# Optimization experiments

Hardware: AMD Instinct MI355X
Metric: run time of the kernel (lower is better)

The kernel has to match this reference:

```python
import jax, jax.numpy as jnp
import numpy as np

GRID = 2
SPAN = 2.0
EMBED = 64
HIDDEN = 128
PRED_LEN = 12
N = 1024
T = 8
SCENE_SIZE = 64


def _social_pool(ht, pos, scene, active):
    """ht: [N,H], pos: [N,2], scene: [N] int, active: [N] bool -> [N, GRID*GRID, H].
    Vectorized equivalent of the per-scene scatter_add pooling: pairwise mask over
    same-scene, active, within-area, non-self pairs; bin neighbor hidden states."""
    n = ht.shape[0]
    half = SPAN / 2.0
    eps = 0.01
    rel = pos[None, :, :] - pos[:, None, :]  # rel[i,j] = pos_j - pos_i
    within = ((rel[..., 0] < half - eps) & (rel[..., 0] > -half + eps)
              & (rel[..., 1] < half - eps) & (rel[..., 1] > -half + eps))
    pair = (within & (~jnp.eye(n, dtype=bool))
            & (scene[:, None] == scene[None, :])
            & active[:, None] & active[None, :])
    cell = SPAN / GRID
    gidx = jnp.floor((rel + half) / cell).astype(jnp.int32)
    gid = jnp.clip(gidx[..., 0] * GRID + gidx[..., 1], 0, GRID * GRID - 1)
    onehot = jax.nn.one_hot(gid, GRID * GRID, dtype=ht.dtype) * pair[..., None].astype(ht.dtype)
    # pooled[i,g,h] = sum_j onehot[i,j,g] * ht[j,h]
    return jnp.einsum('ijg,jh->igh', onehot, ht)


def _lstm_step(x, h, c, Wih, Whh, bih, bhh):
    z = x @ Wih.T + bih + h @ Whh.T + bhh
    i, f, g, o = jnp.split(z, 4, axis=-1)
    c_new = jax.nn.sigmoid(f) * c + jax.nn.sigmoid(i) * jnp.tanh(g)
    h_new = jax.nn.sigmoid(o) * jnp.tanh(c_new)
    return h_new, c_new


def setup_inputs() -> dict:
    key = jax.random.key(0)
    ks = jax.random.split(key, 16)
    past_traj = jax.random.uniform(ks[0], (N, T, 2), dtype=jnp.float32) * 8.0
    past_traj_rel = jax.random.normal(ks[1], (N, T, 2), dtype=jnp.float32)
    past_traj_timestamp_mask = jnp.ones((N, T), dtype=jnp.int32)
    is_predictable = jnp.ones((N, 1), dtype=jnp.int32)
    same_scene_mask = (jnp.arange(N, dtype=jnp.int32) // SCENE_SIZE).reshape(N, 1)

    def lin(k, fan_out, fan_in):
        b = 1.0 / np.sqrt(fan_in)
        return jax.random.uniform(k, (fan_out, fan_in), jnp.float32, -b, b)

    pos_W = lin(ks[2], EMBED, 2)
    pos_b = jnp.zeros((EMBED,), jnp.float32)
    soc_W = lin(ks[3], EMBED, GRID * GRID * HIDDEN)
    soc_b = jnp.zeros((EMBED,), jnp.float32)
    Wih = lin(ks[4], 4 * HIDDEN, 2 * EMBED)
    Whh = lin(ks[5], 4 * HIDDEN, HIDDEN)
    bih = jnp.zeros((4 * HIDDEN,), jnp.float32)
    bhh = jnp.zeros((4 * HIDDEN,), jnp.float32)
    h0 = jax.random.normal(ks[6], (HIDDEN,), jnp.float32) * 0.1
    c0 = jax.random.normal(ks[7], (HIDDEN,), jnp.float32) * 0.1
    pred_W = lin(ks[8], 5, HIDDEN)
    pred_b = jnp.zeros((5,), jnp.float32)
    return {
        'past_traj': past_traj, 'past_traj_rel': past_traj_rel,
        'past_traj_timestamp_mask': past_traj_timestamp_mask,
        'is_predictable': is_predictable, 'same_scene_mask': same_scene_mask,
        'pos_W': pos_W, 'pos_b': pos_b, 'soc_W': soc_W, 'soc_b': soc_b,
        'Wih': Wih, 'Whh': Whh, 'bih': bih, 'bhh': bhh,
        'h0': h0, 'c0': c0, 'pred_W': pred_W, 'pred_b': pred_b,
    }


def reference(past_traj, past_traj_rel, past_traj_timestamp_mask, is_predictable,
              same_scene_mask, pos_W, pos_b, soc_W, soc_b, Wih, Whh, bih, bhh,
              h0, c0, pred_W, pred_b):
    n = past_traj.shape[0]
    scene = same_scene_mask[:, 0]
    ht = jnp.broadcast_to(h0[None, :], (n, HIDDEN))
    ct = jnp.broadcast_to(c0[None, :], (n, HIDDEN))

    def obs_step(carry, inp):
        ht, ct = carry
        point, rel, m = inp  # [N,2], [N,2], [N]
        active = m == 1
        pooled = _social_pool(ht, point, scene, active)  # [N,G^2,H]
        et = jax.nn.relu(rel @ pos_W.T + pos_b)
        at = jax.nn.relu(pooled.reshape(n, -1) @ soc_W.T + soc_b)
        x = jnp.concatenate([et, at], axis=-1)
        h_new, c_new = _lstm_step(x, ht, ct, Wih, Whh, bih, bhh)
        ht = jnp.where(active[:, None], h_new, ht)
        ct = jnp.where(active[:, None], c_new, ct)
        return (ht, ct), None

    obs_inp = (jnp.moveaxis(past_traj, 1, 0), jnp.moveaxis(past_traj_rel, 1, 0),
               jnp.moveaxis(past_traj_timestamp_mask, 1, 0))
    (ht, ct), _ = jax.lax.scan(obs_step, (ht, ct), obs_inp)

    pred_active = past_traj_timestamp_mask[:, -1] == 1
    pos0 = past_traj[:, -1, :]

    def pred_step(carry, _):
        ht, ct, pos = carry
        out = ht @ pred_W.T + pred_b  # [N,5]
        rel = out[:, :2]
        pos = pos + rel
        pooled = _social_pool(ht, pos, scene, pred_active)
        et = jax.nn.relu(rel @ pos_W.T + pos_b)
        at = jax.nn.relu(pooled.reshape(n, -1) @ soc_W.T + soc_b)
        x = jnp.concatenate([et, at], axis=-1)
        h_new, c_new = _lstm_step(x, ht, ct, Wih, Whh, bih, bhh)
        ht = jnp.where(pred_active[:, None], h_new, ht)
        ct = jnp.where(pred_active[:, None], c_new, ct)
        return (ht, ct, pos), (out, pos)

    (_, _, _), (outs, trajs) = jax.lax.scan(pred_step, (ht, ct, pos0), None, length=PRED_LEN)
    pred_out_all = jnp.where(pred_active[:, None, None], jnp.moveaxis(outs, 0, 1), 0.0)
    pred_traj_all = jnp.where(pred_active[:, None, None], jnp.moveaxis(trajs, 0, 1), 0.0)
    # is_predictable is all-ones in this setup, so the final boolean filter is identity
    return pred_out_all, pred_traj_all
```

## Files before the change

kernel.cpp:

```cpp
#include <hip/hip_runtime.h>

#define NAGENT 64
#define HID    128
#define TOBS   8
#define PREDL  12
#define NTHR   1024
#define XP     264
#define PP     264
#define SP2    264

typedef __attribute__((ext_vector_type(8))) short bf16x8;
typedef __attribute__((ext_vector_type(4))) short bf16x4;
typedef __attribute__((ext_vector_type(4))) float f32x4;
typedef __attribute__((ext_vector_type(2))) unsigned int u32x2;

__device__ __forceinline__ unsigned short f2bf(float f) {
    unsigned int x = __float_as_uint(f);
    unsigned int r = (x + 0x7fffu + ((x >> 16) & 1u)) >> 16;
    return (unsigned short)r;
}
__device__ __forceinline__ float bf2f(unsigned short u) {
    return __uint_as_float(((unsigned int)u) << 16);
}
__device__ __forceinline__ float sigmf(float x) {
    return __builtin_amdgcn_rcpf(1.0f + __expf(-x));
}
__device__ __forceinline__ float tanhf_fast(float x) {
    x = fminf(fmaxf(x, -15.0f), 15.0f);
    float e = __expf(2.0f * x);
    return (e - 1.0f) * __builtin_amdgcn_rcpf(e + 1.0f);
}
__device__ __forceinline__ float sel4(float a0, float a1, float a2, float a3, int k) {
    float lo = (k & 1) ? a1 : a0;
    float hi = (k & 1) ? a3 : a2;
    return (k & 2) ? hi : lo;
}

__global__ void prep_weights(const float* __restrict__ Wih, const float* __restrict__ Whh,
                             const float* __restrict__ socW, const float* __restrict__ predW,
                             unsigned short* __restrict__ wd, unsigned short* __restrict__ wb,
                             unsigned short* __restrict__ wp) {
    int idx = blockIdx.x * 256 + threadIdx.x;
    if (idx < 131072) {
        int e = idx & 7, l = (idx >> 3) & 63, t = idx >> 9;
        int kt = t & 7, nt = t >> 3;
        int k = kt * 32 + ((l >> 4) << 3) + e;
        int n = nt * 16 + (l & 15);
        int d = n >> 2, g = n & 3;
        int row = g * 128 + d;
        float v = (k < 128) ? Wih[row * 128 + k] : Whh[row * 128 + (k - 128)];
        wd[idx] = f2bf(v);
    } else if (idx < 163840) {
        int i2 = idx - 131072;
        int e = i2 & 7, l = (i2 >> 3) & 63, t = i2 >> 9;
        int kt = t & 3, nt = t >> 2;
        int k = kt * 32 + ((l >> 4) << 3) + e;
        int r = nt * 16 + (l & 15);
        int eo = r >> 2, g = r & 3;
        wb[i2] = f2bf(socW[eo * 512 + g * 128 + k]);
    } else if (idx < 167936) {
        int i3 = idx - 163840;
        int e = i3 & 7, l = (i3 >> 3) & 63, f = i3 >> 9;
        int kt = f & 3, half = f >> 2;
        int k = kt * 32 + ((l >> 4) << 3) + e;
        int n = l & 15;
        float v = (n < 5) ? predW[n * 128 + k] : 0.0f;
        unsigned short hi = f2bf(v);
        wp[i3] = half ? f2bf(v - bf2f(hi)) : hi;
    }
}

__global__ __launch_bounds__(NTHR) void social_lstm_mfma(
    const float* __restrict__ past_traj, const float* __restrict__ past_traj_rel,
    const int* __restrict__ ts_mask, const int* __restrict__ scene_in,
    const float* __restrict__ pos_W, const float* __restrict__ pos_b,
    const float* __restrict__ soc_b,
    const float* __restrict__ bih, const float* __restrict__ bhh,
    const float* __restrict__ h0, const float* __restrict__ c0,
    const float* __restrict__ pred_b,
    const unsigned short* __restrict__ wd, const unsigned short* __restrict__ wb,
    const unsigned short* __restrict__ wp,
    float* __restrict__ out)
{
    __shared__ __align__(16) unsigned short sh_X[NAGENT][XP];
    __shared__ __align__(16) unsigned short sh_P[NAGENT][PP];
    __shared__ __align__(16) unsigned short sh_S[NAGENT][SP2];
    __shared__ float sh_px[NAGENT], sh_py[NAGENT], sh_rx[NAGENT], sh_ry[NAGENT];
    __shared__ float sh_o[5][NAGENT];
    __shared__ int   sh_act[NAGENT], sh_scene[NAGENT];

    const int tid  = threadIdx.x;
    const int lane = tid & 63;
    const int wv   = __builtin_amdgcn_readfirstlane(tid >> 6);
    const int gbase = blockIdx.x * NAGENT;
    const int c16 = lane & 15;
    const int q4  = lane >> 4;
    const int go  = c16 & 3;
    const int dq  = c16 >> 2;

    float bs[2], c_st[4][2], hnew[4][2];
    int dimv[2];
    #pragma unroll
    for (int s = 0; s < 2; ++s) {
        const int n = (2 * wv + s) * 16 + c16;
        const int d = n >> 2, g = n & 3;
        bs[s] = bih[g * 128 + d] + bhh[g * 128 + d];
        dimv[s] = (2 * wv + s) * 4 + dq;
        #pragma unroll
        for (int mj = 0; mj < 4; ++mj) c_st[mj][s] = c0[dimv[s]];
    }
    for (int p = tid; p < NAGENT * HID; p += NTHR) {
        int a = p >> 7, d = p & 127;
        sh_X[a][128 + d] = f2bf(h0[d]);
    }
    if (tid < NAGENT) sh_scene[tid] = scene_in[gbase + tid];
    __syncthreads();

    const bf16x8* wdp = (const bf16x8*)wd + (2 * wv * 8) * 64 + lane;
    const bf16x8* wbp = (const bf16x8*)wb + (wv * 4) * 64 + lane;
    const unsigned short* xaD = &sh_X[c16][q4 * 8];
    const unsigned short* xaB = &sh_X[c16][128 + q4 * 8];

    for (int step = 0; step < TOBS + PREDL; ++step) {
        if (step < TOBS) {
            if (tid < NAGENT) {
                const int ig = gbase + tid;
                sh_px[tid] = past_traj[(ig * TOBS + step) * 2 + 0];
                sh_py[tid] = past_traj[(ig * TOBS + step) * 2 + 1];
                sh_rx[tid] = past_traj_rel[(ig * TOBS + step) * 2 + 0];
                sh_ry[tid] = past_traj_rel[(ig * TOBS + step) * 2 + 1];
                sh_act[tid] = (ts_mask[ig * TOBS + step] == 1) ? 1 : 0;
            }
        } else {
            if (wv < 4) {
                const bf16x8* wpv = (const bf16x8*)wp;
                f32x4 pa = (f32x4){0.f, 0.f, 0.f, 0.f};
                #pragma unroll
                for (int kt = 0; kt < 4; ++kt) {
                    const bf16x8 a = *(const bf16x8*)&sh_X[wv * 16 + c16][128 + kt * 32 + q4 * 8];
                    pa = __builtin_amdgcn_mfma_f32_16x16x32_bf16(a, wpv[kt * 64 + lane], pa, 0, 0, 0);
                    pa = __builtin_amdgcn_mfma_f32_16x16x32_bf16(a, wpv[(4 + kt) * 64 + lane], pa, 0, 0, 0);
                }
                if (c16 < 5) {
                    const float pb = pred_b[c16];
                    #pragma unroll
                    for (int rr = 0; rr < 4; ++rr)
                        sh_o[c16][wv * 16 + q4 * 4 + rr] = pa[rr] + pb;
                }
            }
            __syncthreads();
            if (tid < NAGENT) {
                const int i = tid;
                const float rx = sh_o[0][i], ry = sh_o[1][i];
                const float px = sh_px[i] + rx, py = sh_py[i] + ry;
                sh_px[i] = px; sh_py[i] = py;
                sh_rx[i] = rx; sh_ry[i] = ry;
                const float m = sh_act[i] ? 1.0f : 0.0f;
                const int p = step - TOBS;
                const int ig = gbase + i;
                float* po = out + (ig * PREDL + p) * 5;
                #pragma unroll
                for (int q = 0; q < 5; ++q) po[q] = m * sh_o[q][i];
                float* pt = out + 61440 + (ig * PREDL + p) * 2;
                pt[0] = m * px; pt[1] = m * py;
            }
        }
        __syncthreads();

        #pragma unroll
        for (int it = 0; it < 4; ++it) {
            const int p = it * NTHR + tid;
            const int i = p >> 6, j = p & 63;
            const float dx = sh_px[j] - sh_px[i];
            const float dy = sh_py[j] - sh_py[i];
            const bool within = (dx < 0.99f) & (dx > -0.99f) & (dy < 0.99f) & (dy > -0.99f);
            const bool pair = within && (i != j) && (sh_scene[i] == sh_scene[j])
                              && sh_act[i] && sh_act[j];
            const int gid = ((dx >= 0.f) ? 2 : 0) + ((dy >= 0.f) ? 1 : 0);
            unsigned int w0 = 0, w1 = 0;
            if (pair) {
                if (gid == 0) w0 = 0x3f80u;
                else if (gid == 1) w0 = 0x3f800000u;
                else if (gid == 2) w1 = 0x3f80u;
                else w1 = 0x3f800000u;
            }
            u32x2 w; w[0] = w0; w[1] = w1;
            *(u32x2*)&sh_P[i][j * 4] = w;
        }
        {
            const float rx = sh_rx[lane], ry = sh_ry[lane];
            const int e0 = wv * 4;
            #pragma unroll
            for (int u = 0; u < 4; ++u) {
                const int e = e0 + u;
                sh_X[lane][e] = f2bf(fmaxf(pos_b[e] + rx * pos_W[e * 2] + ry * pos_W[e * 2 + 1], 0.f));
            }
        }
        {
            f32x4 acc2[4];
            #pragma unroll
            for (int mj = 0; mj < 4; ++mj) acc2[mj] = (f32x4){0.f, 0.f, 0.f, 0.f};
            #pragma unroll
            for (int kt = 0; kt < 4; ++kt) {
                const bf16x8 b = wbp[kt * 64];
                #pragma unroll
                for (int mj = 0; mj < 4; ++mj) {
                    const bf16x8 a = *(const bf16x8*)(xaB + mj * 16 * XP + kt * 32);
                    acc2[mj] = __builtin_amdgcn_mfma_f32_16x16x32_bf16(a, b, acc2[mj], 0, 0, 0);
                }
            }
            const int rcol = wv * 16 + c16;
            #pragma unroll
            for (int mj = 0; mj < 4; ++mj)
                #pragma unroll
                for (int rr = 0; rr < 4; ++rr)
                    sh_S[mj * 16 + q4 * 4 + rr][rcol] = f2bf(acc2[mj][rr]);
        }
        __syncthreads();

        {
            const int mt = wv & 3, nt = wv >> 2;
            const int cb = 4 * (nt * 16 + c16);
            f32x4 cac = (f32x4){0.f, 0.f, 0.f, 0.f};
            #pragma unroll
            for (int kt = 0; kt < 8; ++kt) {
                const bf16x8 a = *(const bf16x8*)&sh_P[mt * 16 + c16][kt * 32 + q4 * 8];
                const int j0 = kt * 8 + q4 * 2;
                const bf16x4 lo = *(const bf16x4*)&sh_S[j0][cb];
                const bf16x4 hi = *(const bf16x4*)&sh_S[j0 + 1][cb];
                const bf16x8 b = __builtin_shufflevector(lo, hi, 0, 1, 2, 3, 4, 5, 6, 7);
                cac = __builtin_amdgcn_mfma_f32_16x16x32_bf16(a, b, cac, 0, 0, 0);
            }
            const int e = nt * 16 + c16;
            const float sb = soc_b[e];
            #pragma unroll
            for (int rr = 0; rr < 4; ++rr)
                sh_X[mt * 16 + q4 * 4 + rr][64 + e] = f2bf(fmaxf(cac[rr] + sb, 0.f));
        }
        __syncthreads();

        {
            f32x4 acc[4][2];
            #pragma unroll
            for (int mj = 0; mj < 4; ++mj) {
                acc[mj][0] = (f32x4){0.f, 0.f, 0.f, 0.f};
                acc[mj][1] = (f32x4){0.f, 0.f, 0.f, 0.f};
            }
            #pragma unroll 2
            for (int kt = 0; kt < 8; ++kt) {
                const bf16x8 b0 = wdp[kt * 64];
                const bf16x8 b1 = wdp[kt * 64 + 512];
                #pragma unroll
                for (int mj = 0; mj < 4; ++mj) {
                    const bf16x8 a = *(const bf16x8*)(xaD + mj * 16 * XP + kt * 32);
                    acc[mj][0] = __builtin_amdgcn_mfma_f32_16x16x32_bf16(a, b0, acc[mj][0], 0, 0, 0);
                    acc[mj][1] = __builtin_amdgcn_mfma_f32_16x16x32_bf16(a, b1, acc[mj][1], 0, 0, 0);
                }
            }
            #pragma unroll
            for (int mj = 0; mj < 4; ++mj) {
                const int a = mj * 16 + q4 * 4 + go;
                const bool act = sh_act[a] != 0;
                #pragma unroll
                for (int s = 0; s < 2; ++s) {
                    const float z0 = acc[mj][s][0] + bs[s];
                    const float z1 = acc[mj][s][1] + bs[s];
                    const float z2 = acc[mj][s][2] + bs[s];
                    const float z3 = acc[mj][s][3] + bs[s];
                    const float s0 = sel4(z0, z1, z2, z3, go);
                    const float s1 = sel4(z0, z1, z2, z3, go ^ 1);
                    const float s2 = sel4(z0, z1, z2, z3, go ^ 2);
                    const float s3 = sel4(z0, z1, z2, z3, go ^ 3);
                    const float t1 = __shfl_xor(s1, 1, 64);
                    const float t2 = __shfl_xor(s2, 2, 64);
                    const float t3 = __shfl_xor(s3, 3, 64);
                    const float zi = sel4(s0, t1, t2, t3, go);
                    const float zf = sel4(s0, t1, t2, t3, go ^ 1);
                    const float zg = sel4(s0, t1, t2, t3, go ^ 2);
                    const float zo = sel4(s0, t1, t2, t3, go ^ 3);
                    const float cold = c_st[mj][s];
                    const float cn = sigmf(zf) * cold + sigmf(zi) * tanhf_fast(zg);
                    const float hn = sigmf(zo) * tanhf_fast(cn);
                    c_st[mj][s] = act ? cn : cold;
                    const float hold = bf2f(sh_X[a][128 + dimv[s]]);
                    hnew[mj][s] = act ? hn : hold;
                }
            }
        }
        __syncthreads();
        #pragma unroll
        for (int mj = 0; mj < 4; ++mj) {
            const int a = mj * 16 + q4 * 4 + go;
            sh_X[a][128 + dimv[0]] = f2bf(hnew[mj][0]);
            sh_X[a][128 + dimv[1]] = f2bf(hnew[mj][1]);
        }
        __syncthreads();
    }
}

extern "C" void kernel_launch(void* const* d_in, const int* in_sizes, int n_in,
                              void* d_out, int out_size, void* d_ws, size_t ws_size,
                              hipStream_t stream) {
    (void)in_sizes; (void)n_in; (void)out_size; (void)ws_size;
    unsigned short* wd = (unsigned short*)d_ws;
    unsigned short* wb = wd + 131072;
    unsigned short* wp = wb + 32768;
    prep_weights<<<656, 256, 0, stream>>>(
        (const float*)d_in[9], (const float*)d_in[10],
        (const float*)d_in[7], (const float*)d_in[15], wd, wb, wp);
    social_lstm_mfma<<<16, NTHR, 0, stream>>>(
        (const float*)d_in[0],
        (const float*)d_in[1],
        (const int*)  d_in[2],
        (const int*)  d_in[4],
        (const float*)d_in[5],
        (const float*)d_in[6],
        (const float*)d_in[8],
        (const float*)d_in[11],
        (const float*)d_in[12],
        (const float*)d_in[13],
        (const float*)d_in[14],
        (const float*)d_in[16],
        wd, wb, wp,
        (float*)d_out);
}
```

Before: 290.2 us.

## Double-buffer hidden state and positions to remove per-step barriers

Splits the hidden state into a double-buffered array so the new h can be written directly after the gate math, dropping the extra barrier and register staging. Position, velocity and activity arrays are double-buffered too, and the next observed step's inputs are prefetched at the end of the current step. The prediction-head writes and position update move into the MFMA waves, removing a separate single-wave phase and another barrier. This adds shared memory and index bookkeeping, and the active-mask handling during prediction relies on buffer 1 holding the last observed mask.

```diff
diff --git a/kernel.cpp b/kernel.cpp
--- a/kernel.cpp
+++ b/kernel.cpp
@@ -5,13 +5,14 @@
 #define TOBS   8
 #define PREDL  12
 #define NTHR   1024
-#define XP     264
+#define XH     136
 #define PP     264
-#define SP2    264
+#define SPP    268
 
 typedef __attribute__((ext_vector_type(8))) short bf16x8;
 typedef __attribute__((ext_vector_type(4))) short bf16x4;
 typedef __attribute__((ext_vector_type(4))) float f32x4;
+typedef __attribute__((ext_vector_type(4))) int   i32x4;
 typedef __attribute__((ext_vector_type(2))) unsigned int u32x2;
 
 __device__ __forceinline__ unsigned short f2bf(float f) {
@@ -82,12 +83,14 @@
     const unsigned short* __restrict__ wp,
     float* __restrict__ out)
 {
-    __shared__ __align__(16) unsigned short sh_X[NAGENT][XP];
+    __shared__ __align__(16) unsigned short sh_X[NAGENT][XH];
+    __shared__ __align__(16) unsigned short sh_H[2][NAGENT][XH];
     __shared__ __align__(16) unsigned short sh_P[NAGENT][PP];
-    __shared__ __align__(16) unsigned short sh_S[NAGENT][SP2];
-    __shared__ float sh_px[NAGENT], sh_py[NAGENT], sh_rx[NAGENT], sh_ry[NAGENT];
-    __shared__ float sh_o[5][NAGENT];
-    __shared__ int   sh_act[NAGENT], sh_scene[NAGENT];
+    __shared__ __align__(16) unsigned short sh_S[NAGENT][SPP];
+    __shared__ float sh_px[2][NAGENT], sh_py[2][NAGENT];
+    __shared__ float sh_rx[2][NAGENT], sh_ry[2][NAGENT];
+    __shared__ __align__(16) int sh_act[2][NAGENT];
+    __shared__ int sh_scene[NAGENT];
 
     const int tid  = threadIdx.x;
     const int lane = tid & 63;
@@ -98,7 +101,7 @@
     const int go  = c16 & 3;
     const int dq  = c16 >> 2;
 
-    float bs[2], c_st[4][2], hnew[4][2];
+    float bs[2], c_st[4][2];
     int dimv[2];
     #pragma unroll
     for (int s = 0; s < 2; ++s) {
@@ -111,71 +114,73 @@
     }
     for (int p = tid; p < NAGENT * HID; p += NTHR) {
         int a = p >> 7, d = p & 127;
-        sh_X[a][128 + d] = f2bf(h0[d]);
-    }
-    if (tid < NAGENT) sh_scene[tid] = scene_in[gbase + tid];
+        sh_H[0][a][d] = f2bf(h0[d]);
+    }
+    if (tid < NAGENT) {
+        const int ig = gbase + tid;
+        sh_scene[tid] = scene_in[ig];
+        sh_px[0][tid] = past_traj[(ig * TOBS + 0) * 2 + 0];
+        sh_py[0][tid] = past_traj[(ig * TOBS + 0) * 2 + 1];
+        sh_rx[0][tid] = past_traj_rel[(ig * TOBS + 0) * 2 + 0];
+        sh_ry[0][tid] = past_traj_rel[(ig * TOBS + 0) * 2 + 1];
+        sh_act[0][tid] = (ts_mask[ig * TOBS + 0] == 1) ? 1 : 0;
+    }
     __syncthreads();
 
     const bf16x8* wdp = (const bf16x8*)wd + (2 * wv * 8) * 64 + lane;
     const bf16x8* wbp = (const bf16x8*)wb + (wv * 4) * 64 + lane;
-    const unsigned short* xaD = &sh_X[c16][q4 * 8];
-    const unsigned short* xaB = &sh_X[c16][128 + q4 * 8];
 
     for (int step = 0; step < TOBS + PREDL; ++step) {
-        if (step < TOBS) {
-            if (tid < NAGENT) {
-                const int ig = gbase + tid;
-                sh_px[tid] = past_traj[(ig * TOBS + step) * 2 + 0];
-                sh_py[tid] = past_traj[(ig * TOBS + step) * 2 + 1];
-                sh_rx[tid] = past_traj_rel[(ig * TOBS + step) * 2 + 0];
-                sh_ry[tid] = past_traj_rel[(ig * TOBS + step) * 2 + 1];
-                sh_act[tid] = (ts_mask[ig * TOBS + step] == 1) ? 1 : 0;
-            }
-        } else {
+        const int pb = step & 1;
+        const int hb = step & 1;
+        const int ab = (step < TOBS) ? pb : 1;
+
+        if (step >= TOBS) {
             if (wv < 4) {
                 const bf16x8* wpv = (const bf16x8*)wp;
                 f32x4 pa = (f32x4){0.f, 0.f, 0.f, 0.f};
                 #pragma unroll
                 for (int kt = 0; kt < 4; ++kt) {
-                    const bf16x8 a = *(const bf16x8*)&sh_X[wv * 16 + c16][128 + kt * 32 + q4 * 8];
+                    const bf16x8 a = *(const bf16x8*)&sh_H[hb][wv * 16 + c16][kt * 32 + q4 * 8];
                     pa = __builtin_amdgcn_mfma_f32_16x16x32_bf16(a, wpv[kt * 64 + lane], pa, 0, 0, 0);
                     pa = __builtin_amdgcn_mfma_f32_16x16x32_bf16(a, wpv[(4 + kt) * 64 + lane], pa, 0, 0, 0);
                 }
                 if (c16 < 5) {
-                    const float pb = pred_b[c16];
+                    const float pbias = pred_b[c16];
+                    const int p = step - TOBS;
+                    const int pprev = (step - 1) & 1;
                     #pragma unroll
-                    for (int rr = 0; rr < 4; ++rr)
-                        sh_o[c16][wv * 16 + q4 * 4 + rr] = pa[rr] + pb;
+                    for (int rr = 0; rr < 4; ++rr) {
+                        const int a = wv * 16 + q4 * 4 + rr;
+                        const float o = pa[rr] + pbias;
+                        const float m = sh_act[1][a] ? 1.0f : 0.0f;
+                        const int ig = gbase + a;
+                        out[(ig * PREDL + p) * 5 + c16] = m * o;
+                        if (c16 == 0) {
+                            const float px = sh_px[pprev][a] + o;
+                            sh_px[pb][a] = px; sh_rx[pb][a] = o;
+                            out[61440 + (ig * PREDL + p) * 2 + 0] = m * px;
+                        }
+                        if (c16 == 1) {
+                            const float py = sh_py[pprev][a] + o;
+                            sh_py[pb][a] = py; sh_ry[pb][a] = o;
+                            out[61440 + (ig * PREDL + p) * 2 + 1] = m * py;
+                        }
+                    }
                 }
             }
             __syncthreads();
-            if (tid < NAGENT) {
-                const int i = tid;
-                const float rx = sh_o[0][i], ry = sh_o[1][i];
-                const float px = sh_px[i] + rx, py = sh_py[i] + ry;
-                sh_px[i] = px; sh_py[i] = py;
-                sh_rx[i] = rx; sh_ry[i] = ry;
-                const float m = sh_act[i] ? 1.0f : 0.0f;
-                const int p = step - TOBS;
-                const int ig = gbase + i;
-                float* po = out + (ig * PREDL + p) * 5;
-                #pragma unroll
-                for (int q = 0; q < 5; ++q) po[q] = m * sh_o[q][i];
-                float* pt = out + 61440 + (ig * PREDL + p) * 2;
-                pt[0] = m * px; pt[1] = m * py;
-            }
-        }
-        __syncthreads();
+        }
 
         #pragma unroll
         for (int it = 0; it < 4; ++it) {
             const int p = it * NTHR + tid;
             const int i = p >> 6, j = p & 63;
-            const float dx = sh_px[j] - sh_px[i];
-            const float dy = sh_py[j] - sh_py[i];
+            const float dx = sh_px[pb][j] - sh_px[pb][i];
+            const float dy = sh_py[pb][j] - sh_py[pb][i];
             const bool within = (dx < 0.99f) & (dx > -0.99f) & (dy < 0.99f) & (dy > -0.99f);
             const bool pair = within && (i != j) && (sh_scene[i] == sh_scene[j])
-                              && sh_act[i] && sh_act[j];
+                              && sh_act[ab][i] && sh_act[ab][j];
             const int gid = ((dx >= 0.f) ? 2 : 0) + ((dy >= 0.f) ? 1 : 0);
             unsigned int w0 = 0, w1 = 0;
             if (pair) {
@@ -188,7 +193,7 @@
             *(u32x2*)&sh_P[i][j * 4] = w;
         }
         {
-            const float rx = sh_rx[lane], ry = sh_ry[lane];
+            const float rx = sh_rx[pb][lane], ry = sh_ry[pb][lane];
             const int e0 = wv * 4;
             #pragma unroll
             for (int u = 0; u < 4; ++u) {
@@ -205,7 +210,7 @@
                 const bf16x8 b = wbp[kt * 64];
                 #pragma unroll
                 for (int mj = 0; mj < 4; ++mj) {
-                    const bf16x8 a = *(const bf16x8*)(xaB + mj * 16 * XP + kt * 32);
+                    const bf16x8 a = *(const bf16x8*)&sh_H[hb][mj * 16 + c16][kt * 32 + q4 * 8];
                     acc2[mj] = __builtin_amdgcn_mfma_f32_16x16x32_bf16(a, b, acc2[mj], 0, 0, 0);
                 }
             }
@@ -252,7 +257,9 @@
                 const bf16x8 b1 = wdp[kt * 64 + 512];
                 #pragma unroll
                 for (int mj = 0; mj < 4; ++mj) {
-                    const bf16x8 a = *(const bf16x8*)(xaD + mj * 16 * XP + kt * 32);
+                    const bf16x8 a = (kt < 4)
+                        ? *(const bf16x8*)&sh_X[mj * 16 + c16][kt * 32 + q4 * 8]
+                        : *(const bf16x8*)&sh_H[hb][mj * 16 + c16][(kt - 4) * 32 + q4 * 8];
                     acc[mj][0] = __builtin_amdgcn_mfma_f32_16x16x32_bf16(a, b0, acc[mj][0], 0, 0, 0);
                     acc[mj][1] = __builtin_amdgcn_mfma_f32_16x16x32_bf16(a, b1, acc[mj][1], 0, 0, 0);
                 }
@@ -260,7 +267,7 @@
             #pragma unroll
             for (int mj = 0; mj < 4; ++mj) {
                 const int a = mj * 16 + q4 * 4 + go;
-                const bool act = sh_act[a] != 0;
+                const bool act = sh_act[ab][a] != 0;
                 #pragma unroll
                 for (int s = 0; s < 2; ++s) {
                     const float z0 = acc[mj][s][0] + bs[s];
@@ -282,17 +289,19 @@
                     const float cn = sigmf(zf) * cold + sigmf(zi) * tanhf_fast(zg);
                     const float hn = sigmf(zo) * tanhf_fast(cn);
                     c_st[mj][s] = act ? cn : cold;
-                    const float hold = bf2f(sh_X[a][128 + dimv[s]]);
-                    hnew[mj][s] = act ? hn : hold;
-                }
-            }
-        }
-        __syncthreads();
-        #pragma unroll
-        for (int mj = 0; mj < 4; ++mj) {
-            const int a = mj * 16 + q4 * 4 + go;
-            sh_X[a][128 + dimv[0]] = f2bf(hnew[mj][0]);
-            sh_X[a][128 + dimv[1]] = f2bf(hnew[mj][1]);
+                    const float hold = bf2f(sh_H[hb][a][dimv[s]]);
+                    sh_H[hb ^ 1][a][dimv[s]] = f2bf(act ? hn : hold);
+                }
+            }
+        }
+        if (step + 1 < TOBS && tid < NAGENT) {
+            const int ig = gbase + tid;
+            const int np = (step + 1) & 1;
+            sh_px[np][tid] = past_traj[(ig * TOBS + step + 1) * 2 + 0];
+            sh_py[np][tid] = past_traj[(ig * TOBS + step + 1) * 2 + 1];
+            sh_rx[np][tid] = past_traj_rel[(ig * TOBS + step + 1) * 2 + 0];
+            sh_ry[np][tid] = past_traj_rel[(ig * TOBS + step + 1) * 2 + 1];
+            sh_act[np][tid] = (ts_mask[ig * TOBS + step + 1] == 1) ? 1 : 0;
         }
         __syncthreads();
     }
```

Result: slower. 299.0 us (+3.1%).
